# Performance work log

Measured on AMD Instinct MI355X. Metric: run time of the kernel, lower is better.

## Reference

```python
import jax, jax.numpy as jnp
import numpy as np

NH, NKV, HD = 32, 8, 64
GROUPS = NH // NKV
NLAYERS, FREQ = 30, 3
NSLOTS = 1 + NLAYERS // FREQ  # 11
LAYER_IDX = 0
TOPK = 128
KB_SCALE = 100.0
PAD = -3.3895313892515355e+38  # torch.finfo(bfloat16).min


def rotate_half(x):
    d = x.shape[-1] // 2
    return jnp.concatenate([-x[..., d:], x[..., :d]], axis=-1)


def apply_rope(x, cos, sin):
    # x: (B, H, S, D); cos/sin: (B, S, D)
    return x * cos[:, None] + rotate_half(x) * sin[:, None]


def setup_inputs() -> dict:
    key = jax.random.key(0)
    ks = jax.random.split(key, 10)
    B, S, H = 2, 1024, 2048
    KBL = 400
    hidden_states = jax.random.normal(ks[0], (B, S, H), jnp.float32)
    # rotary embeddings (LlamaRotaryEmbedding, theta=10000)
    pos = jnp.arange(S, dtype=jnp.float32)
    inv_freq = 1.0 / (10000.0 ** (jnp.arange(0, HD, 2, dtype=jnp.float32) / HD))
    freqs = pos[:, None] * inv_freq[None, :]
    emb = jnp.concatenate([freqs, freqs], axis=-1)  # (S, HD)
    cos = jnp.broadcast_to(jnp.cos(emb)[None], (B, S, HD)).astype(jnp.float32)
    sin = jnp.broadcast_to(jnp.sin(emb)[None], (B, S, HD)).astype(jnp.float32)
    # additive causal mask (B,1,S,S)
    causal = jnp.where(jnp.tril(jnp.ones((S, S), jnp.bool_)), 0.0, PAD).astype(jnp.float32)
    attention_mask = jnp.broadcast_to(causal[None, None], (B, 1, S, S))
    kb_keys = jax.random.normal(ks[1], (KBL, NSLOTS * NH * HD), jnp.float32) * 0.5
    kb_values = jax.random.normal(ks[2], (KBL, NSLOTS * NH * HD), jnp.float32) * 0.5
    s = 0.02
    Wq = jax.random.normal(ks[3], (NH * HD, H), jnp.float32) * s
    Wq2 = jax.random.normal(ks[4], (NH * HD, H), jnp.float32) * s
    Wk = jax.random.normal(ks[5], (NKV * HD, H), jnp.float32) * s
    Wv = jax.random.normal(ks[6], (NKV * HD, H), jnp.float32) * s
    Wo = jax.random.normal(ks[7], (H, NH * HD), jnp.float32) * s
    return {"hidden_states": hidden_states, "cos": cos, "sin": sin,
            "attention_mask": attention_mask, "kb_keys": kb_keys, "kb_values": kb_values,
            "Wq": Wq, "Wq2": Wq2, "Wk": Wk, "Wv": Wv, "Wo": Wo}


def reference(hidden_states, cos, sin, attention_mask, kb_keys, kb_values, Wq, Wq2, Wk, Wv, Wo):
    B, S, H = hidden_states.shape
    scale = 1.0 / jnp.sqrt(jnp.float32(HD))

    # projections (attention_bias=False)
    q = (hidden_states @ Wq.T).reshape(B, S, NH, HD).transpose(0, 2, 1, 3)
    q2 = (hidden_states @ Wq2.T).reshape(B, S, NH, HD).transpose(0, 2, 1, 3)
    k = (hidden_states @ Wk.T).reshape(B, S, NKV, HD).transpose(0, 2, 1, 3)
    v = (hidden_states @ Wv.T).reshape(B, S, NKV, HD).transpose(0, 2, 1, 3)

    q = apply_rope(q, cos, sin)
    k = apply_rope(k, cos, sin)

    # repeat_kv (GQA)
    k = jnp.repeat(k, GROUPS, axis=1)  # (B, NH, S, HD)
    v = jnp.repeat(v, GROUPS, axis=1)

    # KB slot select (layer_idx % freq == 0, kb_idx = layer_idx // freq = 0)
    KBL = kb_keys.shape[0]
    kb_idx = LAYER_IDX // FREQ
    kbk = kb_keys.reshape(KBL, NSLOTS, NH * HD)[:, kb_idx].reshape(KBL, NH, HD).transpose(1, 0, 2)
    kbv = kb_values.reshape(KBL, NSLOTS, NH * HD)[:, kb_idx].reshape(KBL, NH, HD).transpose(1, 0, 2)
    kbk = jnp.broadcast_to(kbk[None], (B, NH, KBL, HD))
    kbv = jnp.broadcast_to(kbv[None], (B, NH, KBL, HD))

    # dynamic_sparsify: prune_key_value
    aw_kb = jnp.einsum('bhsd,bhkd->bhsk', q2, kbk) * scale  # (B,NH,S,KBL)
    scores = aw_kb.sum(axis=(1, 2))  # (B, KBL)
    top_idx = jax.lax.stop_gradient(jax.lax.top_k(scores, TOPK)[1])  # (B, TOPK)
    idx = jnp.broadcast_to(top_idx[:, None, :, None], (B, NH, TOPK, HD))
    kbk_g = jax.lax.stop_gradient(jnp.take_along_axis(kbk, idx, axis=2))  # gather under no_grad
    kbv_g = jax.lax.stop_gradient(jnp.take_along_axis(kbv, idx, axis=2))
    aw2 = aw_kb[..., :TOPK]  # source slices (not gathers) the first topk columns

    key_states = jnp.concatenate([kbk_g, k], axis=2)  # (B,NH,TOPK+S,HD)
    value_states = jnp.concatenate([kbv_g, v], axis=2)

    # KB attention mask block
    padding = jnp.all(attention_mask < 0, axis=-1, keepdims=True)  # (B,1,S,1)
    kb_mask = jnp.where(padding, PAD, 0.0).astype(attention_mask.dtype)
    kb_mask = jnp.broadcast_to(kb_mask, (B, 1, S, TOPK))
    mask = jnp.concatenate([kb_mask, attention_mask], axis=-1)  # (B,1,S,TOPK+S)

    aw = jnp.einsum('bhsd,bhkd->bhsk', q, key_states) * scale
    # seperate_query_head: replace KB block with q2-based scores (with kb scale shift)
    aw_seq = aw[..., TOPK:]
    aw2 = aw2 - np.log(TOPK) + np.log(KB_SCALE)
    aw = jnp.concatenate([aw2, aw_seq], axis=-1)

    aw = aw + mask[:, :, :, :key_states.shape[2]]
    aw = jax.nn.softmax(aw.astype(jnp.float32), axis=-1).astype(q.dtype)

    attn = jnp.einsum('bhsk,bhkd->bhsd', aw, value_states)  # (B,NH,S,HD)
    attn = attn.transpose(0, 2, 1, 3).reshape(B, S, NH * HD)
    return attn @ Wo.T
```

## Files before the change

### kernel.cpp

```cpp
#include <hip/hip_runtime.h>
#include <hip/hip_bf16.h>
#include <math.h>

#define NH 32
#define NKV 8
#define HD 64
#define NSLOTS 11
#define TOPK 128
#define KBROW (NSLOTS * NH * HD)
#define PADF (-3.3895313892515355e+38f)
#define C0F  (-0.24686007793152578f)
#define SCALE 0.125f
#define HCH 32

typedef __attribute__((ext_vector_type(8))) __bf16 bf16x8;
typedef __attribute__((ext_vector_type(8))) unsigned short u16x8;
typedef __attribute__((ext_vector_type(4))) float f32x4;

#define GLDS16(gp, lp)                                                        \
  __builtin_amdgcn_global_load_lds(                                           \
      (__attribute__((address_space(1))) void*)(gp),                          \
      (__attribute__((address_space(3))) void*)(lp), 16, 0, 0)

__device__ __forceinline__ unsigned short f2bf(float f) {
  unsigned int u = __float_as_uint(f);
  u = (u + 0x7fffu + ((u >> 16) & 1u)) >> 16;
  return (unsigned short)u;
}

__device__ __forceinline__ int swz(int row, int chunk) {
  return row * 128 + ((chunk ^ (row & 7)) << 4);
}

__global__ void f2bf_all(const float* __restrict__ s0, const float* __restrict__ s1,
                         const float* __restrict__ s2, const float* __restrict__ s3,
                         const float* __restrict__ s4, const float* __restrict__ s5,
                         int n0, int n1, int n2, int n3, int n4_, int n5,
                         unsigned short* __restrict__ out) {
  int i = blockIdx.x * blockDim.x + threadIdx.x;
  int j = i;
  const float* src;
  if (j < n0) src = s0;
  else { j -= n0; if (j < n1) src = s1;
  else { j -= n1; if (j < n2) src = s2;
  else { j -= n2; if (j < n3) src = s3;
  else { j -= n3; if (j < n4_) src = s4;
  else { j -= n4_; if (j >= n5) return; src = s5; }}}}}
  float4 v = ((const float4*)src)[j];
  ushort4 o = {f2bf(v.x), f2bf(v.y), f2bf(v.z), f2bf(v.w)};
  ((ushort4*)out)[i] = o;
}

__global__ __launch_bounds__(256) void gemm_nt_splitk(
    const unsigned short* __restrict__ A, const unsigned short* __restrict__ B,
    float* __restrict__ C0, float* __restrict__ C1, int M, int N, int K) {
  __shared__ unsigned short ldsA[128 * 32];
  __shared__ unsigned short ldsB[128 * 32];
  const int t = threadIdx.x;
  const int l = t & 63, w = t >> 6;
  const int wr = w >> 1, wc = w & 1;
  const int lr = l & 15;
  const int kb = (l >> 4) * 16;
  const int bm = blockIdx.y * 128, bn = blockIdx.x * 128;
  float* C = blockIdx.z ? C1 : C0;
  const int k0base = blockIdx.z * (K >> 1);
  const int kend = k0base + (K >> 1);

  f32x4 acc[4][4] = {};

  for (int k0 = k0base; k0 < kend; k0 += 32) {
    __syncthreads();
#pragma unroll
    for (int it = 0; it < 2; ++it) {
      int s = it * 256 + t;
      int row = s >> 2, cs = (s & 3) * 8;
      GLDS16(A + (size_t)(bm + row) * K + k0 + cs,
             (char*)ldsA + (it * 4 + w) * 1024);
      GLDS16(B + (size_t)(bn + row) * K + k0 + cs,
             (char*)ldsB + (it * 4 + w) * 1024);
    }
    __syncthreads();

    bf16x8 a[4], b[4];
#pragma unroll
    for (int m = 0; m < 4; ++m)
      a[m] = *(const bf16x8*)((const char*)ldsA +
                              (wr * 64 + m * 16 + lr) * 64 + kb);
#pragma unroll
    for (int n = 0; n < 4; ++n)
      b[n] = *(const bf16x8*)((const char*)ldsB +
                              (wc * 64 + n * 16 + lr) * 64 + kb);
#pragma unroll
    for (int m = 0; m < 4; ++m)
#pragma unroll
      for (int n = 0; n < 4; ++n)
        acc[m][n] =
            __builtin_amdgcn_mfma_f32_16x16x32_bf16(a[m], b[n], acc[m][n], 0, 0, 0);
  }

#pragma unroll
  for (int m = 0; m < 4; ++m)
#pragma unroll
    for (int n = 0; n < 4; ++n) {
      int rbase = bm + wr * 64 + m * 16 + ((l >> 4) << 2);
      int cbase = bn + wc * 64 + n * 16 + lr;
#pragma unroll
      for (int j = 0; j < 4; ++j)
        C[(size_t)(rbase + j) * N + cbase] = acc[m][n][j];
    }
}

__global__ void add2_kernel(const float* __restrict__ a,
                            const float* __restrict__ b,
                            float* __restrict__ o, int n4) {
  int i = blockIdx.x * blockDim.x + threadIdx.x;
  if (i >= n4) return;
  float4 x = ((const float4*)a)[i], y = ((const float4*)b)[i];
  ((float4*)o)[i] = make_float4(x.x + y.x, x.y + y.y, x.z + y.z, x.w + y.w);
}

__global__ __launch_bounds__(512) void gemm_proj8(
    const unsigned short* __restrict__ A,
    const unsigned short* __restrict__ Wall,
    const float* __restrict__ cosb, const float* __restrict__ sinb,
    unsigned short* __restrict__ qbf, unsigned short* __restrict__ q2bf,
    unsigned short* __restrict__ kbf, unsigned short* __restrict__ vTb,
    int M, int K, int S) {
  __shared__ char lds[131072];
  const int t = threadIdx.x;
  const int w = t >> 6;
  const int wm = w >> 2, wn = w & 3;
  const int l = t & 63;
  const int li = l & 15, lg4 = l >> 4;
  const int bm = blockIdx.y * 256, bn = blockIdx.x * 256;
  const int NK = K >> 6;

  f32x4 acc[8][4] = {};

#define STAGE_UNIT(kt1, nb, u)                                                \
  {                                                                           \
    const int slice_ = (u) >> 1;                                              \
    const unsigned short* mat_ = ((u) & 1) ? Wall : A;                        \
    const int tb_ = ((u) & 1) ? bn : bm;                                      \
    char* base_ = lds + (nb) * 65536 + (((u) & 1) ? 32768 : 0) +              \
                  slice_ * 16384;                                             \
    _Pragma("unroll")                                                         \
    for (int i_ = 0; i_ < 2; ++i_) {                                          \
      int ss_ = i_ * 512 + t;                                                 \
      int row_ = ss_ >> 2, cc_ = ss_ & 3;                                     \
      int chunk_ = cc_ ^ ((row_ >> 1) & 3);                                   \
      GLDS16(mat_ + (size_t)(tb_ + row_) * K + (kt1) * 64 + slice_ * 32 +     \
                 chunk_ * 8,                                                  \
             base_ + i_ * 8192 + w * 1024);                                   \
    }                                                                         \
  }

  STAGE_UNIT(0, 0, 0); STAGE_UNIT(0, 0, 1);
  STAGE_UNIT(0, 0, 2); STAGE_UNIT(0, 0, 3);
  asm volatile("s_waitcnt vmcnt(4)" ::: "memory");
  asm volatile("s_barrier" ::: "memory");

  for (int kt = 0; kt < NK; ++kt) {
    const int cur = kt & 1;
    const bool stg = (kt + 1 < NK);
    char* curA = lds + cur * 65536;
    char* curB = curA + 32768;
#pragma unroll
    for (int kk = 0; kk < 2; ++kk) {
      bf16x8 bfr[4], af_a[4], af_b[4];
#pragma unroll
      for (int n = 0; n < 4; ++n) {
        int row = wn * 64 + n * 16 + li;
        bfr[n] = *(const bf16x8*)(curB + kk * 16384 + row * 64 +
                                  ((lg4 ^ ((row >> 1) & 3)) << 4));
      }
#pragma unroll
      for (int mi = 0; mi < 4; ++mi) {
        int row = wm * 128 + mi * 16 + li;
        af_a[mi] = *(const bf16x8*)(curA + kk * 16384 + row * 64 +
                                    ((lg4 ^ ((row >> 1) & 3)) << 4));
      }
      if (stg) STAGE_UNIT(kt + 1, cur ^ 1, kk * 2)
#pragma unroll
      for (int mi = 0; mi < 4; ++mi) {
        int row = wm * 128 + (4 + mi) * 16 + li;
        af_b[mi] = *(const bf16x8*)(curA + kk * 16384 + row * 64 +
                                    ((lg4 ^ ((row >> 1) & 3)) << 4));
      }
      __builtin_amdgcn_s_setprio(1);
#pragma unroll
      for (int mi = 0; mi < 4; ++mi)
#pragma unroll
        for (int n = 0; n < 4; ++n)
          acc[mi][n] = __builtin_amdgcn_mfma_f32_16x16x32_bf16(
              af_a[mi], bfr[n], acc[mi][n], 0, 0, 0);
      __builtin_amdgcn_s_setprio(0);
      if (stg) STAGE_UNIT(kt + 1, cur ^ 1, kk * 2 + 1)
      __builtin_amdgcn_s_setprio(1);
#pragma unroll
      for (int mi = 0; mi < 4; ++mi)
#pragma unroll
        for (int n = 0; n < 4; ++n)
          acc[4 + mi][n] = __builtin_amdgcn_mfma_f32_16x16x32_bf16(
              af_b[mi], bfr[n], acc[4 + mi][n], 0, 0, 0);
      __builtin_amdgcn_s_setprio(0);
      if (kk == 0) {
        if (kt == NK - 1) asm volatile("s_waitcnt vmcnt(0)" ::: "memory");
        else              asm volatile("s_waitcnt vmcnt(4)" ::: "memory");
        asm volatile("s_barrier" ::: "memory");
      } else {
        if (stg) {
          asm volatile("s_waitcnt vmcnt(4)" ::: "memory");
          asm volatile("s_barrier" ::: "memory");
        }
      }
    }
  }
#undef STAGE_UNIT

  const int seg = bn;
#pragma unroll
  for (int m = 0; m < 8; ++m) {
    const int row0 = bm + wm * 128 + m * 16 + lg4 * 4;
    if (seg < 2048 || (seg >= 4096 && seg < 4608)) {
      const bool isq = seg < 2048;
#pragma unroll
      for (int j = 0; j < 4; ++j) {
        int row = row0 + j;
        const float* cr = cosb + (size_t)row * 64;
        const float* sr = sinb + (size_t)row * 64;
        float c0 = cr[li], c1 = cr[16 + li], c2 = cr[32 + li], c3 = cr[48 + li];
        float sa = sr[li], sb = sr[16 + li], sc_ = sr[32 + li], sd = sr[48 + li];
        float x0 = acc[m][0][j], x1 = acc[m][1][j];
        float x2 = acc[m][2][j], x3 = acc[m][3][j];
        float y0 = x0 * c0 - x2 * sa;
        float y1 = x1 * c1 - x3 * sb;
        float y2 = x2 * c2 + x0 * sc_;
        float y3 = x3 * c3 + x1 * sd;
        if (isq) {
          size_t ro = (size_t)row * 2048 + bn + wn * 64 + li;
          qbf[ro] = f2bf(y0); qbf[ro + 16] = f2bf(y1);
          qbf[ro + 32] = f2bf(y2); qbf[ro + 48] = f2bf(y3);
        } else {
          size_t ro = (size_t)row * 512 + (bn - 4096) + wn * 64 + li;
          kbf[ro] = f2bf(y0); kbf[ro + 16] = f2bf(y1);
          kbf[ro + 32] = f2bf(y2); kbf[ro + 48] = f2bf(y3);
        }
      }
    } else if (seg < 4096) {
#pragma unroll
      for (int n = 0; n < 4; ++n) {
        int col = bn - 2048 + wn * 64 + n * 16 + li;
#pragma unroll
        for (int j = 0; j < 4; ++j)
          q2bf[(size_t)(row0 + j) * 2048 + col] = f2bf(acc[m][n][j]);
      }
    } else {
      int b_ = row0 / S, s = row0 % S;
#pragma unroll
      for (int n = 0; n < 4; ++n) {
        int col = (bn - 4608) + wn * 64 + n * 16 + li;
        int gg = col >> 6, d = col & 63;
        ushort4 o = {f2bf(acc[m][n][0]), f2bf(acc[m][n][1]),
                     f2bf(acc[m][n][2]), f2bf(acc[m][n][3])};
        *(ushort4*)&vTb[(((size_t)b_ * NKV + gg) * 64 + d) * S + s] = o;
      }
    }
  }
}

__global__ void kbkh_kernel(const float* __restrict__ kbk,
                            unsigned short* __restrict__ out) {
  int i = blockIdx.x * blockDim.x + threadIdx.x;
  if (i >= 128 * 512) return;
  int j = i >> 9, c4 = (i & 511) * 4;
  float4 v = *(const float4*)&kbk[(size_t)j * KBROW + c4];
  ushort4 o = {f2bf(v.x), f2bf(v.y), f2bf(v.z), f2bf(v.w)};
  *(ushort4*)&out[(size_t)j * 2048 + c4] = o;
}

__global__ __launch_bounds__(256) void kbvgt_kernel(
    const float* __restrict__ kbv, const int* __restrict__ topi,
    unsigned short* __restrict__ kbvgT, int B) {
  int h = blockIdx.x % NH, b = blockIdx.x / NH;
  __shared__ unsigned short gt[128][72];
  __shared__ int lidx[TOPK];
  int t = threadIdx.x;
  if (t < TOPK) lidx[t] = topi[b * TOPK + t];
  __syncthreads();
#pragma unroll
  for (int it = 0; it < 8; ++it) {
    int slot = it * 256 + t;
    int j = slot >> 4, d4 = (slot & 15) * 4;
    float4 v = *(const float4*)&kbv[(size_t)lidx[j] * KBROW + h * 64 + d4];
    gt[j][d4] = f2bf(v.x); gt[j][d4 + 1] = f2bf(v.y);
    gt[j][d4 + 2] = f2bf(v.z); gt[j][d4 + 3] = f2bf(v.w);
  }
  __syncthreads();
#pragma unroll
  for (int it = 0; it < 4; ++it) {
    int slot = it * 256 + t;
    int d = slot >> 4, j8 = (slot & 15) * 8;
    u16x8 o;
#pragma unroll
    for (int j = 0; j < 8; ++j) o[j] = gt[j8 + j][d];
    *(u16x8*)&kbvgT[(((size_t)b * NH + h) * 64 + d) * 128 + j8] = o;
  }
}

__global__ __launch_bounds__(256) void hsum1_kernel(
    const float* __restrict__ hidden, double* __restrict__ part,
    int B, int S, int H) {
  const int nhb = H >> 8;
  int hb = blockIdx.x % nhb;
  int ch = (blockIdx.x / nhb) % HCH;
  int b  = blockIdx.x / (nhb * HCH);
  int c  = hb * 256 + threadIdx.x;
  int rows = S / HCH;
  const float* p = hidden + ((size_t)b * S + (size_t)ch * rows) * H + c;
  double acc = 0.0;
  for (int s = 0; s < rows; ++s) acc += (double)p[(size_t)s * H];
  part[((size_t)b * HCH + ch) * H + c] = acc;
}

__global__ void hsum2_kernel(const double* __restrict__ part,
                             float* __restrict__ Hsum, int B, int H) {
  int idx = blockIdx.x * blockDim.x + threadIdx.x;
  if (idx >= B * H) return;
  int b = idx / H, c = idx % H;
  const double* p = part + (size_t)b * HCH * H + c;
  double acc = 0.0;
#pragma unroll
  for (int ch = 0; ch < HCH; ++ch) acc += p[(size_t)ch * H];
  Hsum[idx] = (float)acc;
}

__global__ void qs_kernel(const float* __restrict__ Hsum,
                          const float* __restrict__ Wq2,
                          float* __restrict__ Qs, int B, int H) {
  int task = (blockIdx.x * blockDim.x + threadIdx.x) >> 6;
  int lane = threadIdx.x & 63;
  if (task >= B * NH * HD) return;
  int b = task / (NH * HD), c = task % (NH * HD);
  const float* hs = Hsum + (size_t)b * H;
  const float* wr = Wq2 + (size_t)c * H;
  double acc = 0.0;
  for (int k = lane; k < H; k += 64) acc += (double)hs[k] * (double)wr[k];
#pragma unroll
  for (int off = 32; off; off >>= 1) acc += __shfl_xor(acc, off);
  if (lane == 0) Qs[task] = (float)acc;
}

__global__ void scores_kernel(const float* __restrict__ Qs,
                              const float* __restrict__ kbk,
                              float* __restrict__ scores, int B, int KBL) {
  int task = (blockIdx.x * blockDim.x + threadIdx.x) >> 6;
  int lane = threadIdx.x & 63;
  if (task >= B * KBL) return;
  int b = task / KBL, l = task % KBL;
  const float* kr = kbk + (size_t)l * KBROW;
  const float* qd = Qs + (size_t)b * NH * HD;
  double acc = 0.0;
  for (int c = lane; c < NH * HD; c += 64) acc += (double)qd[c] * (double)kr[c];
#pragma unroll
  for (int off = 32; off; off >>= 1) acc += __shfl_xor(acc, off);
  if (lane == 0) scores[task] = (float)(0.125 * acc);
}

__global__ __launch_bounds__(256) void topk_kernel(
    const float* __restrict__ scores, int* __restrict__ top_idx, int KBL) {
  __shared__ float ls[512];
  int b = blockIdx.x, t = threadIdx.x;
  for (int i = t; i < KBL; i += 256) ls[i] = scores[(size_t)b * KBL + i];
  __syncthreads();
  for (int l = t; l < KBL; l += 256) {
    float sl = ls[l];
    int rank = 0;
    for (int j = 0; j < KBL; ++j) {
      float sj = ls[j];
      rank += (sj > sl || (sj == sl && j < l)) ? 1 : 0;
    }
    if (rank < TOPK) top_idx[b * TOPK + rank] = l;
  }
}

__global__ void padflag_kernel(const float* __restrict__ mask,
                               int* __restrict__ flags, int BS, int S) {
  int w = (blockIdx.x * blockDim.x + threadIdx.x) >> 6;
  int lane = threadIdx.x & 63;
  if (w >= BS) return;
  const float* row = mask + (size_t)w * S;
  bool ok = true;
  for (int j = lane; j < S; j += 64) ok = ok && (row[j] < 0.f);
  int allv = __all(ok ? 1 : 0);
  if (lane == 0) flags[w] = allv;
}

__device__ __forceinline__ void load_chunk(
    int ch, int t, int b, int h, int g, int S,
    const unsigned short* __restrict__ kbf, const unsigned short* __restrict__ vTb,
    const unsigned short* __restrict__ kbkh, const unsigned short* __restrict__ kbvgT,
    bf16x8* st) {
  bool iskb = ch < 2;
  int j0 = iskb ? ch * 64 : (ch - 2) * 64;
#pragma unroll
  for (int it = 0; it < 4; ++it) {
    int slot = it * 256 + t;
    int tile = slot >> 9, row = (slot >> 3) & 63, ck = slot & 7;
    const unsigned short* src;
    if (tile == 0)
      src = iskb ? kbkh + (size_t)(j0 + row) * 2048 + h * 64 + ck * 8
                 : kbf + (size_t)(b * S + j0 + row) * 512 + g * 64 + ck * 8;
    else
      src = iskb ? kbvgT + (((size_t)b * NH + h) * 64 + row) * 128 + j0 + ck * 8
                 : vTb + (((size_t)b * NKV + g) * 64 + row) * (size_t)S + j0 + ck * 8;
    st[it] = *(const bf16x8*)src;
  }
}

__device__ __forceinline__ void attn_step(
    const char* smem, char* ptw, const int* padfb, const bf16x8* aq,
    bool iskb, int j0, int s0, int w, int li, int lg4,
    float* m_, float* l_, f32x4* acc) {
  f32x4 cc[4];
  __builtin_amdgcn_s_setprio(1);
#pragma unroll
  for (int cb = 0; cb < 4; ++cb) {
    bf16x8 b0 = *(const bf16x8*)(smem + swz(cb * 16 + li, lg4));
    bf16x8 b1 = *(const bf16x8*)(smem + swz(cb * 16 + li, 4 + lg4));
    f32x4 z = {};
    z = __builtin_amdgcn_mfma_f32_16x16x32_bf16(aq[0], b0, z, 0, 0, 0);
    z = __builtin_amdgcn_mfma_f32_16x16x32_bf16(aq[1], b1, z, 0, 0, 0);
    cc[cb] = z;
  }
  __builtin_amdgcn_s_setprio(0);

  float lgv[4][4];
#pragma unroll
  for (int cb = 0; cb < 4; ++cb)
#pragma unroll
    for (int j = 0; j < 4; ++j) {
      float v = SCALE * cc[cb][j];
      if (iskb) {
        v += C0F + (padfb[w * 16 + lg4 * 4 + j] ? PADF : 0.f);
      } else {
        int key = j0 + cb * 16 + li;
        int srow = s0 + w * 16 + lg4 * 4 + j;
        v += (key <= srow) ? 0.f : PADF;
      }
      lgv[cb][j] = v;
    }
#pragma unroll
  for (int j = 0; j < 4; ++j) {
    float rmax = fmaxf(fmaxf(lgv[0][j], lgv[1][j]), fmaxf(lgv[2][j], lgv[3][j]));
#pragma unroll
    for (int off = 8; off; off >>= 1) rmax = fmaxf(rmax, __shfl_xor(rmax, off));
    float mn = fmaxf(m_[j], rmax);
    float fs = __expf(m_[j] - mn);
    float csum = 0.f;
#pragma unroll
    for (int cb = 0; cb < 4; ++cb) {
      float pv = __expf(lgv[cb][j] - mn);
      csum += pv;
      int key = cb * 16 + li;
      int rloc = lg4 * 4 + j;
      *(unsigned short*)(ptw + swz(rloc, key >> 3) + ((key & 7) << 1)) = f2bf(pv);
    }
#pragma unroll
    for (int off = 8; off; off >>= 1) csum += __shfl_xor(csum, off);
    m_[j] = mn;
    l_[j] = l_[j] * fs + csum;
#pragma unroll
    for (int db = 0; db < 4; ++db) acc[db][j] *= fs;
  }

  bf16x8 pa0 = *(const bf16x8*)(ptw + swz(li, lg4));
  bf16x8 pa1 = *(const bf16x8*)(ptw + swz(li, 4 + lg4));
  __builtin_amdgcn_s_setprio(1);
#pragma unroll
  for (int db = 0; db < 4; ++db) {
    bf16x8 bv0 = *(const bf16x8*)(smem + 8192 + swz(db * 16 + li, lg4));
    bf16x8 bv1 = *(const bf16x8*)(smem + 8192 + swz(db * 16 + li, 4 + lg4));
    acc[db] = __builtin_amdgcn_mfma_f32_16x16x32_bf16(pa0, bv0, acc[db], 0, 0, 0);
    acc[db] = __builtin_amdgcn_mfma_f32_16x16x32_bf16(pa1, bv1, acc[db], 0, 0, 0);
  }
  __builtin_amdgcn_s_setprio(0);
}

__global__ __launch_bounds__(256) void attn_mfma(
    const unsigned short* __restrict__ qbf,
    const unsigned short* __restrict__ q2bf,
    const unsigned short* __restrict__ kbf,
    const unsigned short* __restrict__ vTb,
    const unsigned short* __restrict__ kbkh,
    const unsigned short* __restrict__ kbvgT,
    const int* __restrict__ padflag,
    unsigned short* __restrict__ attnbf,
    int B, int S) {
  const int nst = S >> 6;
  const int npair = (nst + 1) >> 1;
  const int p = blockIdx.x % npair;
  const int h = (blockIdx.x / npair) % NH;
  const int b = blockIdx.x / (npair * NH);
  const int stA = p, stB = nst - 1 - p;
  const bool hasB = (stB != stA);
  const int s0A = stA * 64, s0B = stB * 64;
  const int g = h / (NH / NKV);

  __shared__ unsigned short smem[8192];
  __shared__ unsigned short pt[4][1024];
  __shared__ int padf[128];

  const int t = threadIdx.x;
  const int w = t >> 6;
  const int li = t & 15;
  const int lg4 = (t & 63) >> 4;

  const int nch = 2 + stB + 1;

  bf16x8 st[4];
  load_chunk(0, t, b, h, g, S, kbf, vTb, kbkh, kbvgT, st);

  bf16x8 aq0A[2], aq2A[2], aq0B[2], aq2B[2];
  {
    size_t rowA = (size_t)(b * S + s0A + w * 16 + li) * (NH * HD);
    size_t rowB = (size_t)(b * S + s0B + w * 16 + li) * (NH * HD);
#pragma unroll
    for (int kc = 0; kc < 2; ++kc) {
      size_t o = h * 64 + kc * 32 + lg4 * 8;
      aq0A[kc] = *(const bf16x8*)(qbf + rowA + o);
      aq2A[kc] = *(const bf16x8*)(q2bf + rowA + o);
      aq0B[kc] = *(const bf16x8*)(qbf + rowB + o);
      aq2B[kc] = *(const bf16x8*)(q2bf + rowB + o);
    }
  }
  if (t < 64) padf[t] = padflag[b * S + s0A + t];
  else if (t < 128) padf[t] = padflag[b * S + s0B + (t - 64)];

  float mA[4] = {-3.4e38f, -3.4e38f, -3.4e38f, -3.4e38f};
  float mB[4] = {-3.4e38f, -3.4e38f, -3.4e38f, -3.4e38f};
  float lA[4] = {}, lB[4] = {};
  f32x4 accA[4] = {}, accB[4] = {};

  for (int ch = 0; ch < nch; ++ch) {
    const bool iskb = ch < 2;
    const int j0 = iskb ? ch * 64 : (ch - 2) * 64;
    if (ch) __syncthreads();
#pragma unroll
    for (int it = 0; it < 4; ++it) {
      int slot = it * 256 + t;
      int tile = slot >> 9, row = (slot >> 3) & 63, ck = slot & 7;
      *(bf16x8*)((char*)smem + tile * 8192 + swz(row, ck)) = st[it];
    }
    __syncthreads();
    if (ch + 1 < nch) load_chunk(ch + 1, t, b, h, g, S, kbf, vTb, kbkh, kbvgT, st);

    if (iskb || (ch - 2) <= stA)
      attn_step((const char*)smem, (char*)pt[w], padf, iskb ? aq2A : aq0A,
                iskb, j0, s0A, w, li, lg4, mA, lA, accA);
    if (hasB)
      attn_step((const char*)smem, (char*)pt[w], padf + 64, iskb ? aq2B : aq0B,
                iskb, j0, s0B, w, li, lg4, mB, lB, accB);
  }

#pragma unroll
  for (int j = 0; j < 4; ++j) {
    float inv = 1.f / lA[j];
    size_t o = (size_t)(b * S + s0A + w * 16 + lg4 * 4 + j) * (NH * HD) + h * 64 + li;
#pragma unroll
    for (int db = 0; db < 4; ++db) attnbf[o + db * 16] = f2bf(accA[db][j] * inv);
  }
  if (hasB) {
#pragma unroll
    for (int j = 0; j < 4; ++j) {
      float inv = 1.f / lB[j];
      size_t o = (size_t)(b * S + s0B + w * 16 + lg4 * 4 + j) * (NH * HD) + h * 64 + li;
#pragma unroll
      for (int db = 0; db < 4; ++db) attnbf[o + db * 16] = f2bf(accB[db][j] * inv);
    }
  }
}

extern "C" void kernel_launch(void* const* d_in, const int* in_sizes, int n_in,
                              void* d_out, int out_size, void* d_ws, size_t ws_size,
                              hipStream_t stream) {
  const float* hidden = (const float*)d_in[0];
  const float* cosb   = (const float*)d_in[1];
  const float* sinb   = (const float*)d_in[2];
  const float* mask   = (const float*)d_in[3];
  const float* kbk    = (const float*)d_in[4];
  const float* kbv    = (const float*)d_in[5];
  const float* Wq     = (const float*)d_in[6];
  const float* Wq2    = (const float*)d_in[7];
  const float* Wk     = (const float*)d_in[8];
  const float* Wv     = (const float*)d_in[9];
  const float* Wo     = (const float*)d_in[10];
  float* out = (float*)d_out;

  const int H   = in_sizes[6] / (NH * HD);
  const int KBL = in_sizes[4] / KBROW;
  const long long BSll = (long long)in_sizes[0] / H;
  const int S = (int)((long long)in_sizes[3] / BSll);
  const int B = (int)(BSll / S);
  const int BS = B * S;
  const int NQ = NH * HD;
  const int NKVD = NKV * HD;
  const int NTOT = NQ + NQ + NKVD + NKVD;

  float* ws = (float*)d_ws;
  size_t off = 0;
  double* hpart = (double*)(ws + off); off += (size_t)B * HCH * H * 2;
  float* Hsum = ws + off; off += (size_t)B * H;
  float* Qs   = ws + off; off += (size_t)B * NQ;
  float* sc   = ws + off; off += (size_t)B * KBL;
  int* topi   = (int*)(ws + off); off += (size_t)B * TOPK;
  int* padfl  = (int*)(ws + off); off += (size_t)BS;
  unsigned short* hbf    = (unsigned short*)(ws + off); off += (size_t)BS * H / 2;
  unsigned short* wall   = (unsigned short*)(ws + off); off += (size_t)NTOT * H / 2;
  unsigned short* wobf   = (unsigned short*)(ws + off); off += (size_t)H * NQ / 2;
  unsigned short* attnbf = (unsigned short*)(ws + off); off += (size_t)BS * NQ / 2;
  unsigned short* qbf    = (unsigned short*)(ws + off); off += (size_t)BS * NQ / 2;
  unsigned short* q2bf   = (unsigned short*)(ws + off); off += (size_t)BS * NQ / 2;
  unsigned short* kbf    = (unsigned short*)(ws + off); off += (size_t)BS * NKVD / 2;
  unsigned short* vTb    = (unsigned short*)(ws + off); off += (size_t)BS * NKVD / 2;
  unsigned short* kbkh   = (unsigned short*)(ws + off); off += (size_t)128 * NQ / 2;
  unsigned short* kbvgT  = (unsigned short*)(ws + off); off += (size_t)B * NH * HD * TOPK / 2;
  float* c0 = (float*)qbf;
  float* c1 = (float*)wall;
  (void)ws_size; (void)n_in; (void)out_size;

  {
    int n0 = BS * H / 4, n1 = NQ * H / 4, n2 = NQ * H / 4;
    int n3 = NKVD * H / 4, n4_ = NKVD * H / 4, n5 = H * NQ / 4;
    int ntot = n0 + n1 + n2 + n3 + n4_ + n5;
    f2bf_all<<<(ntot + 255) / 256, 256, 0, stream>>>(
        hidden, Wq, Wq2, Wk, Wv, Wo, n0, n1, n2, n3, n4_, n5, hbf);
  }

  gemm_proj8<<<dim3(NTOT / 256, BS / 256), 512, 0, stream>>>(
      hbf, wall, cosb, sinb, qbf, q2bf, kbf, vTb, BS, H, S);

  hsum1_kernel<<<B * HCH * (H / 256), 256, 0, stream>>>(hidden, hpart, B, S, H);
  hsum2_kernel<<<(B * H + 255) / 256, 256, 0, stream>>>(hpart, Hsum, B, H);
  qs_kernel<<<(B * NQ * 64 + 255) / 256, 256, 0, stream>>>(Hsum, Wq2, Qs, B, H);
  scores_kernel<<<(B * KBL * 64 + 255) / 256, 256, 0, stream>>>(Qs, kbk, sc, B, KBL);
  topk_kernel<<<B, 256, 0, stream>>>(sc, topi, KBL);
  padflag_kernel<<<(BS * 64 + 255) / 256, 256, 0, stream>>>(mask, padfl, BS, S);

  kbkh_kernel<<<(128 * 512 + 255) / 256, 256, 0, stream>>>(kbk, kbkh);
  kbvgt_kernel<<<B * NH, 256, 0, stream>>>(kbv, topi, kbvgT, B);

  {
    int nst = S / 64;
    int npair = (nst + 1) / 2;
    attn_mfma<<<B * NH * npair, 256, 0, stream>>>(
        qbf, q2bf, kbf, vTb, kbkh, kbvgT, padfl, attnbf, B, S);
  }

  gemm_nt_splitk<<<dim3(H / 128, BS / 128, 2), 256, 0, stream>>>(
      attnbf, wobf, c0, c1, BS, H, NQ);
  add2_kernel<<<(BS * H / 4 + 255) / 256, 256, 0, stream>>>(c0, c1, out, BS * H / 4);
}
```

Baseline: 256.2 us.

## Fuse hidden bf16 conversion into column-sum kernel, remap GEMM blocks, drop setprio

The fp32-to-bf16 conversion of hidden_states moves out of the bulk conversion kernel and into the column-sum kernel, which already reads hidden. This removes one full pass over the activations, and the column-sum kernel now runs before the projection GEMM. The projection GEMM also remaps workgroup IDs in groups of 8, which looks aimed at chiplet or L2 locality, and drops the s_setprio wrapping around its MFMA blocks. Risks: the column-sum kernel writes bf16 with a strided per-thread pattern, which may be less efficient than the vectorized conversion it replaces, and the remap assumes the grid size divides by 8.

After: 250.4 us. 2.3% less time.

```diff
diff --git a/kernel.cpp b/kernel.cpp
--- a/kernel.cpp
+++ b/kernel.cpp
@@ -34,8 +34,8 @@
 
 __global__ void f2bf_all(const float* __restrict__ s0, const float* __restrict__ s1,
                          const float* __restrict__ s2, const float* __restrict__ s3,
-                         const float* __restrict__ s4, const float* __restrict__ s5,
-                         int n0, int n1, int n2, int n3, int n4_, int n5,
+                         const float* __restrict__ s4,
+                         int n0, int n1, int n2, int n3, int n4_,
                          unsigned short* __restrict__ out) {
   int i = blockIdx.x * blockDim.x + threadIdx.x;
   int j = i;
@@ -44,8 +44,7 @@
   else { j -= n0; if (j < n1) src = s1;
   else { j -= n1; if (j < n2) src = s2;
   else { j -= n2; if (j < n3) src = s3;
-  else { j -= n3; if (j < n4_) src = s4;
-  else { j -= n4_; if (j >= n5) return; src = s5; }}}}}
+  else { j -= n3; if (j >= n4_) return; src = s4; }}}}
   float4 v = ((const float4*)src)[j];
   ushort4 o = {f2bf(v.x), f2bf(v.y), f2bf(v.z), f2bf(v.w)};
   ((ushort4*)out)[i] = o;
@@ -132,7 +131,11 @@
   const int wm = w >> 2, wn = w & 3;
   const int l = t & 63;
   const int li = l & 15, lg4 = l >> 4;
-  const int bm = blockIdx.y * 256, bn = blockIdx.x * 256;
+  const int nwgx = gridDim.x;
+  const int cpx = (nwgx * gridDim.y) >> 3;
+  int linear = blockIdx.x + nwgx * blockIdx.y;
+  int wid = (linear & 7) * cpx + (linear >> 3);
+  const int bm = (wid / nwgx) * 256, bn = (wid % nwgx) * 256;
   const int NK = K >> 6;
 
   f32x4 acc[8][4] = {};
@@ -187,23 +190,19 @@
         af_b[mi] = *(const bf16x8*)(curA + kk * 16384 + row * 64 +
                                     ((lg4 ^ ((row >> 1) & 3)) << 4));
       }
-      __builtin_amdgcn_s_setprio(1);
 #pragma unroll
       for (int mi = 0; mi < 4; ++mi)
 #pragma unroll
         for (int n = 0; n < 4; ++n)
           acc[mi][n] = __builtin_amdgcn_mfma_f32_16x16x32_bf16(
               af_a[mi], bfr[n], acc[mi][n], 0, 0, 0);
-      __builtin_amdgcn_s_setprio(0);
       if (stg) STAGE_UNIT(kt + 1, cur ^ 1, kk * 2 + 1)
-      __builtin_amdgcn_s_setprio(1);
 #pragma unroll
       for (int mi = 0; mi < 4; ++mi)
 #pragma unroll
         for (int n = 0; n < 4; ++n)
           acc[4 + mi][n] = __builtin_amdgcn_mfma_f32_16x16x32_bf16(
               af_b[mi], bfr[n], acc[4 + mi][n], 0, 0, 0);
-      __builtin_amdgcn_s_setprio(0);
       if (kk == 0) {
         if (kt == NK - 1) asm volatile("s_waitcnt vmcnt(0)" ::: "memory");
         else              asm volatile("s_waitcnt vmcnt(4)" ::: "memory");
@@ -310,16 +309,21 @@
 
 __global__ __launch_bounds__(256) void hsum1_kernel(
     const float* __restrict__ hidden, double* __restrict__ part,
-    int B, int S, int H) {
+    unsigned short* __restrict__ hbf, int B, int S, int H) {
   const int nhb = H >> 8;
   int hb = blockIdx.x % nhb;
   int ch = (blockIdx.x / nhb) % HCH;
   int b  = blockIdx.x / (nhb * HCH);
   int c  = hb * 256 + threadIdx.x;
   int rows = S / HCH;
-  const float* p = hidden + ((size_t)b * S + (size_t)ch * rows) * H + c;
+  size_t base = ((size_t)b * S + (size_t)ch * rows) * H + c;
+  const float* p = hidden + base;
   double acc = 0.0;
-  for (int s = 0; s < rows; ++s) acc += (double)p[(size_t)s * H];
+  for (int s = 0; s < rows; ++s) {
+    float v = p[(size_t)s * H];
+    acc += (double)v;
+    hbf[base + (size_t)s * H] = f2bf(v);
+  }
   part[((size_t)b * HCH + ch) * H + c] = acc;
 }
 
@@ -630,17 +634,18 @@
   (void)ws_size; (void)n_in; (void)out_size;
 
   {
-    int n0 = BS * H / 4, n1 = NQ * H / 4, n2 = NQ * H / 4;
+    int n1 = NQ * H / 4, n2 = NQ * H / 4;
     int n3 = NKVD * H / 4, n4_ = NKVD * H / 4, n5 = H * NQ / 4;
-    int ntot = n0 + n1 + n2 + n3 + n4_ + n5;
+    int ntot = n1 + n2 + n3 + n4_ + n5;
     f2bf_all<<<(ntot + 255) / 256, 256, 0, stream>>>(
-        hidden, Wq, Wq2, Wk, Wv, Wo, n0, n1, n2, n3, n4_, n5, hbf);
-  }
+        Wq, Wq2, Wk, Wv, Wo, n1, n2, n3, n4_, n5, wall);
+  }
+
+  hsum1_kernel<<<B * HCH * (H / 256), 256, 0, stream>>>(hidden, hpart, hbf, B, S, H);
 
   gemm_proj8<<<dim3(NTOT / 256, BS / 256), 512, 0, stream>>>(
       hbf, wall, cosb, sinb, qbf, q2bf, kbf, vTb, BS, H, S);
 
-  hsum1_kernel<<<B * HCH * (H / 256), 256, 0, stream>>>(hidden, hpart, B, S, H);
   hsum2_kernel<<<(B * H + 255) / 256, 256, 0, stream>>>(hpart, Hsum, B, H);
   qs_kernel<<<(B * NQ * 64 + 255) / 256, 256, 0, stream>>>(Hsum, Wq2, Qs, B, H);
   scores_kernel<<<(B * KBL * 64 + 255) / 256, 256, 0, stream>>>(Qs, kbk, sc, B, KBL);
```
